# Kernel optimization log

Measured on AMD Instinct MI355X. Metric: run time of the kernel, lower is better.

Reference implementation:

```python
import jax, jax.numpy as jnp
import numpy as np

HIDDEN = 512
CTX = 768
B, N, M = 8, 4096, 1024


def setup_inputs() -> dict:
    key = jax.random.key(0)
    ks = jax.random.split(key, 7)
    s = lambda fan_in: 1.0 / np.sqrt(fan_in)
    return {
        "x": jax.random.normal(ks[0], (B, N, HIDDEN), jnp.float32),
        "context": jax.random.normal(ks[1], (B, M, CTX), jnp.float32),
        "Wq": jax.random.normal(ks[2], (HIDDEN, HIDDEN), jnp.float32) * s(HIDDEN),
        "bq": jnp.zeros((HIDDEN,), jnp.float32),
        "Wk": jax.random.normal(ks[3], (CTX, HIDDEN), jnp.float32) * s(CTX),
        "bk": jnp.zeros((HIDDEN,), jnp.float32),
        "Wv": jax.random.normal(ks[4], (CTX, HIDDEN), jnp.float32) * s(CTX),
        "bv": jnp.zeros((HIDDEN,), jnp.float32),
        "Wo": jax.random.normal(ks[5], (HIDDEN, HIDDEN), jnp.float32) * s(HIDDEN),
        "bo": jnp.zeros((HIDDEN,), jnp.float32),
    }


def reference(x, context, Wq, bq, Wk, bk, Wv, bv, Wo, bo):
    scale = HIDDEN ** (-0.5)
    q = jnp.einsum("bnd,de->bne", x, Wq) + bq          # [B,N,H]
    k = jnp.einsum("bmc,ce->bme", context, Wk) + bk    # [B,M,H]
    v = jnp.einsum("bmc,ce->bme", context, Wv) + bv    # [B,M,H]
    scores = jnp.einsum("bne,bme->bnm", q, k) * scale  # [B,N,M]
    attn = jax.nn.softmax(scores, axis=-1)
    ctx_out = jnp.einsum("bnm,bme->bne", attn, v)      # [B,N,H]
    out = jnp.einsum("bne,ed->bnd", ctx_out, Wo) + bo
    return out + x
```

## Files before the change

### kernel.cpp

```cpp
#include <hip/hip_runtime.h>

typedef __attribute__((ext_vector_type(8))) short short8;
typedef __attribute__((ext_vector_type(4))) float f32x4;
typedef __attribute__((ext_vector_type(4))) int i32x4;

#define NSEQ 4096
#define MSEQ 1024
#define HID  512
#define CTXD 768

static __device__ __forceinline__ unsigned short f2bf(float f) {
  union { float f; unsigned u; } v; v.f = f;
  return (unsigned short)((v.u + 0x7fffu + ((v.u >> 16) & 1u)) >> 16);
}
static __device__ __forceinline__ float bf2f(unsigned short u) {
  union { unsigned u; float f; } v; v.u = ((unsigned)u) << 16;
  return v.f;
}

static __device__ __forceinline__ void gld16(const void* g, void* l) {
  __builtin_amdgcn_global_load_lds((const __attribute__((address_space(1))) void*)g,
                                   (__attribute__((address_space(3))) void*)l, 16, 0, 0);
}

__global__ void k_transpose(const float* __restrict__ W, unsigned short* __restrict__ WT,
                            int K, int N) {
  __shared__ float tile[32][33];
  int k0 = blockIdx.x * 32, n0 = blockIdx.y * 32;
  int tx = threadIdx.x, ty = threadIdx.y;
#pragma unroll
  for (int i = 0; i < 32; i += 8)
    tile[ty + i][tx] = W[(size_t)(k0 + ty + i) * N + n0 + tx];
  __syncthreads();
#pragma unroll
  for (int i = 0; i < 32; i += 8)
    WT[(size_t)(n0 + ty + i) * K + k0 + tx] = f2bf(tile[tx][ty + i]);
}

__global__ void k_cast(const float* __restrict__ in, unsigned short* __restrict__ out, int n8) {
  int i = blockIdx.x * blockDim.x + threadIdx.x;
  int stride = gridDim.x * blockDim.x;
  for (; i < n8; i += stride) {
    f32x4 v0 = *(const f32x4*)(in + (size_t)i * 8);
    f32x4 v1 = *(const f32x4*)(in + (size_t)i * 8 + 4);
    unsigned short tmp[8] __attribute__((aligned(16)));
    tmp[0] = f2bf(v0[0]); tmp[1] = f2bf(v0[1]); tmp[2] = f2bf(v0[2]); tmp[3] = f2bf(v0[3]);
    tmp[4] = f2bf(v1[0]); tmp[5] = f2bf(v1[1]); tmp[6] = f2bf(v1[2]); tmp[7] = f2bf(v1[3]);
    *(i32x4*)(out + (size_t)i * 8) = *(const i32x4*)tmp;
  }
}

template<int BIAS_MODE, bool RES, bool OUT_BF16, int ZMODE>
__global__ __launch_bounds__(256, 2) void k_gemm(
    const unsigned short* __restrict__ A, const unsigned short* __restrict__ B,
    const float* __restrict__ bias, const float* __restrict__ resv,
    void* __restrict__ Cv, int M, int N, int K,
    long sA, long sB, long sC, long sR) {
  __shared__ __align__(16) char lds[65536];
  const int t = threadIdx.x, lane = t & 63, wid = t >> 6;
  const int wr = wid >> 1, wc = wid & 1;
  int m0, n0, z;
  if (ZMODE == 2) {
    int bid = blockIdx.x; z = bid & 7; int r = bid >> 3;
    m0 = (r >> 3) * 128; n0 = (r & 7) * 128;
  } else {
    m0 = blockIdx.x * 128; n0 = blockIdx.y * 128; z = blockIdx.z;
  }
  const unsigned short* Ab = A + (size_t)z * sA;
  const unsigned short* Bb = B + (size_t)z * sB;

  const f32x4 fz = {0.f, 0.f, 0.f, 0.f};
  f32x4 acc[4][4];
#pragma unroll
  for (int i = 0; i < 4; i++)
#pragma unroll
    for (int j = 0; j < 4; j++) acc[i][j] = fz;

  const int srow = t >> 3;
  const int schunk = t & 7;

  auto stage = [&](int kk, int buf) {
    const char* a8 = (const char*)Ab;
    const char* b8 = (const char*)Bb;
#pragma unroll
    for (int i = 0; i < 4; i++) {
      int row = i * 32 + srow;
      gld16(a8 + ((size_t)(m0 + row) * K + kk) * 2 + ((schunk ^ (row & 7)) << 4),
            lds + buf * 32768 + i * 4096 + wid * 1024);
    }
#pragma unroll
    for (int i = 0; i < 4; i++) {
      int row = i * 32 + srow;
      gld16(b8 + ((size_t)(n0 + row) * K + kk) * 2 + ((schunk ^ (row & 7)) << 4),
            lds + buf * 32768 + 16384 + i * 4096 + wid * 1024);
    }
  };

  stage(0, 0);
  int buf = 0;
  for (int kk = 0; kk < K; kk += 64) {
    if (kk + 64 < K) {
      stage(kk + 64, buf ^ 1);
      asm volatile("s_waitcnt vmcnt(8)" ::: "memory");
    } else {
      asm volatile("s_waitcnt vmcnt(0)" ::: "memory");
    }
    __builtin_amdgcn_s_barrier();
    const char* As = lds + buf * 32768;
    const char* Bs = As + 16384;
#pragma unroll
    for (int ks = 0; ks < 2; ks++) {
      short8 af[4], bfr[4];
#pragma unroll
      for (int i = 0; i < 4; i++) {
        int r = wr * 64 + i * 16 + (lane & 15);
        af[i] = *(const short8*)(As + r * 128 +
                 (((unsigned)(ks * 64 + (lane >> 4) * 16)) ^ ((unsigned)(r & 7) << 4)));
      }
#pragma unroll
      for (int i = 0; i < 4; i++) {
        int r = wc * 64 + i * 16 + (lane & 15);
        bfr[i] = *(const short8*)(Bs + r * 128 +
                 (((unsigned)(ks * 64 + (lane >> 4) * 16)) ^ ((unsigned)(r & 7) << 4)));
      }
#pragma unroll
      for (int i = 0; i < 4; i++)
#pragma unroll
        for (int j = 0; j < 4; j++)
          acc[i][j] = __builtin_amdgcn_mfma_f32_16x16x32_bf16(af[i], bfr[j], acc[i][j], 0, 0, 0);
    }
    asm volatile("s_waitcnt lgkmcnt(0)" ::: "memory");
    __builtin_amdgcn_s_barrier();
    buf ^= 1;
  }

  const float* res = RES ? (resv + (size_t)z * sR) : nullptr;
  char* Cb = (char*)Cv + (size_t)z * sC * (OUT_BF16 ? 2 : 4);
#pragma unroll
  for (int i = 0; i < 4; i++) {
#pragma unroll
    for (int jj = 0; jj < 4; jj++) {
      int row = m0 + wr * 64 + i * 16 + (lane >> 4) * 4 + jj;
#pragma unroll
      for (int j = 0; j < 4; j++) {
        int col = n0 + wc * 64 + j * 16 + (lane & 15);
        float v = acc[i][j][jj];
        if (BIAS_MODE == 1) v += bias[col];
        if (BIAS_MODE == 2) v += bias[row];
        if (RES) v += res[(size_t)row * N + col];
        if (OUT_BF16) ((unsigned short*)Cb)[(size_t)row * N + col] = f2bf(v);
        else          ((float*)Cb)[(size_t)row * N + col] = v;
      }
    }
  }
}

template<int BIAS_MODE, bool RES, bool OUT_BF16, int ZMODE, int EPI, bool AF32>
__global__ __launch_bounds__(512, 1) void k_gemm3(
    const unsigned short* __restrict__ A, const unsigned short* __restrict__ B,
    const float* __restrict__ bias, const float* __restrict__ resv,
    void* __restrict__ Cv, int M, int N, int K,
    long sA, long sB, long sC, long sR,
    const float* __restrict__ ps, float* __restrict__ psout) {
  __shared__ __align__(16) char lds[99328];
  const int t = threadIdx.x, lane = t & 63, wid = t >> 6;
  const int wr = wid >> 2, wc = wid & 3;
  const int l15 = lane & 15, g = lane >> 4;
  int m0, n0, z;
  if (ZMODE == 1) {
    int bid = blockIdx.x; z = bid & 7; int r = bid >> 3;
    m0 = (r >> 1) * 256; n0 = (r & 1) * 256;
  } else if (ZMODE == 3) {
    int bid = blockIdx.x; z = bid & 7; int r = bid >> 3;
    m0 = (r >> 2) * 256; n0 = (r & 3) * 256;
  } else {
    m0 = blockIdx.x * 256; n0 = blockIdx.y * 256; z = blockIdx.z;
  }
  const unsigned short* Ab = A + (size_t)z * sA;
  const float* Af = (const float*)A + (size_t)z * sA;
  const unsigned short* Bb = B + (size_t)z * sB;

  float* invb = (float*)(lds + 98304);
  if (EPI == 2) {
    if (t < 256) {
      size_t rr = (size_t)z * 4096 + (m0 + t);
      invb[t] = 1.0f / (ps[rr] + ps[32768 + rr] + ps[65536 + rr] + ps[98304 + rr]);
    }
    __syncthreads();
  }

  const f32x4 fz = {0.f, 0.f, 0.f, 0.f};
  f32x4 acc[8][4];
#pragma unroll
  for (int i = 0; i < 8; i++)
#pragma unroll
    for (int j = 0; j < 4; j++) acc[i][j] = fz;

  int rS[2], cS[2];
#pragma unroll
  for (int u = 0; u < 2; u++) {
    int p = u * 8192 + wid * 1024 + lane * 16;
    int L = p >> 7;
    int q = (p & 127) ^ ((L & 7) << 4);
    rS[u] = 2 * L + (q >> 6);
    cS[u] = q & 63;
  }

  auto stageA = [&](int kk, int buf, int u) {
    gld16((const char*)Ab + ((size_t)(m0 + rS[u]) * K + kk) * 2 + cS[u],
          lds + buf * 32768 + u * 8192 + wid * 1024);
  };
  auto stageB = [&](int kk, int buf, int u) {
    gld16((const char*)Bb + ((size_t)(n0 + rS[u]) * K + kk) * 2 + cS[u],
          lds + buf * 32768 + 16384 + u * 8192 + wid * 1024);
  };

  f32x4 araw[2][2];
  auto loadAraw = [&](int kk) {
#pragma unroll
    for (int u = 0; u < 2; u++) {
      const float* src = Af + (size_t)(m0 + rS[u]) * K + kk + (cS[u] >> 1);
      araw[u][0] = *(const f32x4*)(src);
      araw[u][1] = *(const f32x4*)(src + 4);
    }
  };
  auto writeA = [&](int buf) {
#pragma unroll
    for (int u = 0; u < 2; u++) {
      unsigned short tmp[8] __attribute__((aligned(16)));
#pragma unroll
      for (int e = 0; e < 4; e++) tmp[e] = f2bf(araw[u][0][e]);
#pragma unroll
      for (int e = 0; e < 4; e++) tmp[4 + e] = f2bf(araw[u][1][e]);
      *(i32x4*)(lds + buf * 32768 + u * 8192 + wid * 1024 + lane * 16) = *(const i32x4*)tmp;
    }
  };

  auto ldso = [&](int r, int gg) -> unsigned {
    unsigned L = (unsigned)(r >> 1);
    return L * 128 + ((((unsigned)(r & 1)) * 64 + (unsigned)gg * 16) ^ ((L & 7) << 4));
  };

  const int NT = K >> 5;
  if (AF32) {
    loadAraw(0);
#pragma unroll
    for (int u = 0; u < 2; u++) stageB(0, 0, u);
    writeA(0);
    loadAraw(32);
#pragma unroll
    for (int u = 0; u < 2; u++) stageB(32, 1, u);
    writeA(1);
  } else {
#pragma unroll
    for (int u = 0; u < 2; u++) { stageA(0, 0, u); }
#pragma unroll
    for (int u = 0; u < 2; u++) { stageB(0, 0, u); }
#pragma unroll
    for (int u = 0; u < 2; u++) { stageA(32, 1, u); }
#pragma unroll
    for (int u = 0; u < 2; u++) { stageB(32, 1, u); }
  }

  for (int tt = 0; tt < NT; tt++) {
    if (AF32) {
      asm volatile("s_waitcnt vmcnt(0)" ::: "memory");
    } else if (tt + 1 < NT) {
      asm volatile("s_waitcnt vmcnt(4)" ::: "memory");
    } else {
      asm volatile("s_waitcnt vmcnt(0)" ::: "memory");
    }
    __builtin_amdgcn_s_barrier();
    asm volatile("" ::: "memory");
    const char* As = lds + (tt % 3) * 32768;
    const char* Bs = As + 16384;
    const int kk2 = (tt + 2) << 5;
    const bool st = kk2 < K;
    const int bn = (tt + 2) % 3;

    if (AF32 && st) loadAraw(kk2);

    short8 bfr[4], af[8];
#pragma unroll
    for (int fj = 0; fj < 4; fj++) {
      int r = wc * 64 + fj * 16 + l15;
      bfr[fj] = *(const short8*)(Bs + ldso(r, g));
    }
#pragma unroll
    for (int fi = 0; fi < 8; fi++) {
      int r = wr * 128 + fi * 16 + l15;
      af[fi] = *(const short8*)(As + ldso(r, g));
    }
    if (!AF32 && st) { stageA(kk2, bn, 0); stageA(kk2, bn, 1); stageB(kk2, bn, 0); stageB(kk2, bn, 1); }
    __builtin_amdgcn_s_setprio(1);
#pragma unroll
    for (int fi = 0; fi < 8; fi++)
#pragma unroll
      for (int fj = 0; fj < 4; fj++)
        acc[fi][fj] =
            __builtin_amdgcn_mfma_f32_16x16x32_bf16(af[fi], bfr[fj], acc[fi][fj], 0, 0, 0);
    __builtin_amdgcn_s_setprio(0);
    if (AF32 && st) { writeA(bn); stageB(kk2, bn, 0); stageB(kk2, bn, 1); }
    asm volatile("" ::: "memory");
  }
  asm volatile("s_waitcnt lgkmcnt(0)" ::: "memory");
  __builtin_amdgcn_s_barrier();
  asm volatile("" ::: "memory");

  char* Cb = (char*)Cv + (size_t)z * sC * (OUT_BF16 ? 2 : 4);

  if (EPI == 1) {
    const float scale = 0.044194173824159216f;
    float* redb = (float*)lds;
#pragma unroll
    for (int i = 0; i < 8; i++) {
#pragma unroll
      for (int jj = 0; jj < 4; jj++) {
        int rl = wr * 128 + i * 16 + g * 4 + jj;
        int row = m0 + rl;
        float e4 = 0.f;
#pragma unroll
        for (int j = 0; j < 4; j++) {
          int col = n0 + wc * 64 + j * 16 + l15;
          float e = __expf(acc[i][j][jj] * scale);
          unsigned short h = f2bf(e);
          ((unsigned short*)Cb)[(size_t)row * N + col] = h;
          e4 += bf2f(h);
        }
#pragma unroll
        for (int d = 1; d < 16; d <<= 1) e4 += __shfl_xor(e4, d, 64);
        if (l15 == 0) redb[wc * 256 + rl] = e4;
      }
    }
    __syncthreads();
    if (t < 256) {
      float s4 = redb[t] + redb[256 + t] + redb[512 + t] + redb[768 + t];
      psout[(size_t)(n0 >> 8) * 32768 + (size_t)z * 4096 + (m0 + t)] = s4;
    }
    return;
  }

  const float* res = RES ? (resv + (size_t)z * sR) : nullptr;
#pragma unroll
  for (int i = 0; i < 8; i++) {
#pragma unroll
    for (int jj = 0; jj < 4; jj++) {
      int rl = wr * 128 + i * 16 + g * 4 + jj;
      int row = m0 + rl;
      float inv = 1.0f;
      if (EPI == 2) inv = invb[rl];
#pragma unroll
      for (int j = 0; j < 4; j++) {
        int col = n0 + wc * 64 + j * 16 + l15;
        float v = acc[i][j][jj];
        if (EPI == 2) v *= inv;
        if (BIAS_MODE == 1) v += bias[col];
        if (BIAS_MODE == 2) v += bias[row];
        if (RES) v += res[(size_t)row * N + col];
        if (OUT_BF16) ((unsigned short*)Cb)[(size_t)row * N + col] = f2bf(v);
        else          ((float*)Cb)[(size_t)row * N + col] = v;
      }
    }
  }
}

extern "C" void kernel_launch(void* const* d_in, const int* in_sizes, int n_in,
                              void* d_out, int out_size, void* d_ws, size_t ws_size,
                              hipStream_t stream) {
  (void)in_sizes; (void)n_in; (void)out_size; (void)ws_size;
  const float* x   = (const float*)d_in[0];
  const float* ctx = (const float*)d_in[1];
  const float* Wq  = (const float*)d_in[2];
  const float* bq  = (const float*)d_in[3];
  const float* Wk  = (const float*)d_in[4];
  const float* bk  = (const float*)d_in[5];
  const float* Wv  = (const float*)d_in[6];
  const float* bv  = (const float*)d_in[7];
  const float* Wo  = (const float*)d_in[8];
  const float* bo  = (const float*)d_in[9];
  float* out = (float*)d_out;

  char* ws = (char*)d_ws;
  unsigned short* qb   = (unsigned short*)(ws);
  unsigned short* kbuf = (unsigned short*)(ws + 33554432);
  unsigned short* Vb   = (unsigned short*)(ws + 41943040);
  unsigned short* UT   = (unsigned short*)(ws + 50331648);
  unsigned short* WqT  = (unsigned short*)(ws + 58720256);
  unsigned short* WkT  = (unsigned short*)(ws + 59244544);
  unsigned short* WvT  = (unsigned short*)(ws + 60030976);
  unsigned short* WoT  = (unsigned short*)(ws + 60817408);
  unsigned short* cb   = (unsigned short*)(ws + 61341696);
  unsigned short* Sbuf = (unsigned short*)(ws + 73924608);
  float* psums = (float*)(ws + 141033472);

  dim3 tb(32, 8);
  k_transpose<<<dim3(16, 16), tb, 0, stream>>>(Wq, WqT, 512, 512);
  k_transpose<<<dim3(24, 16), tb, 0, stream>>>(Wk, WkT, 768, 512);
  k_transpose<<<dim3(24, 16), tb, 0, stream>>>(Wv, WvT, 768, 512);
  k_transpose<<<dim3(16, 16), tb, 0, stream>>>(Wo, WoT, 512, 512);

  k_cast<<<dim3(2048), 256, 0, stream>>>(ctx, cb, 786432);

  k_gemm3<1, false, true, 0, 0, true><<<dim3(128, 2, 1), 512, 0, stream>>>(
      (const unsigned short*)x, WqT, bq, nullptr, qb, 32768, 512, 512,
      0, 0, 0, 0, nullptr, nullptr);
  k_gemm<1, false, true, 0><<<dim3(64, 4, 1), 256, 0, stream>>>(
      cb, WkT, bk, nullptr, kbuf, 8192, 512, 768, 0, 0, 0, 0);
  k_gemm<1, false, true, 0><<<dim3(64, 4, 1), 256, 0, stream>>>(
      cb, WvT, bv, nullptr, Vb, 8192, 512, 768, 0, 0, 0, 0);
  k_gemm<0, false, true, 2><<<dim3(256), 256, 0, stream>>>(
      WoT, Vb, nullptr, nullptr, UT, 512, 1024, 512,
      0, (long)1024 * 512, (long)512 * 1024, 0);
  k_gemm3<0, false, true, 3, 1, false><<<dim3(512), 512, 0, stream>>>(
      qb, kbuf, nullptr, nullptr, Sbuf, 4096, 1024, 512,
      (long)4096 * 512, (long)1024 * 512, (long)4096 * 1024, 0, nullptr, psums);
  k_gemm3<1, true, false, 1, 2, false><<<dim3(256), 512, 0, stream>>>(
      Sbuf, UT, bo, x, out, 4096, 512, 1024,
      (long)4096 * 1024, (long)512 * 1024, (long)4096 * 512, (long)4096 * 512,
      psums, nullptr);
}
```

Before: 185.1 us.

## Fuse K/V projections into one fp32-input GEMM and batch weight transposes

Merges the four weight-transpose launches into one z-indexed kernel and drops the separate context bf16 cast kernel. The K and V projections become a single 256-tile GEMM that reads fp32 context directly and writes an interleaved [B*M,1024] K|V buffer. A leading-dimension parameter (ldb) is added so downstream GEMMs can read K and V out of that interleaved buffer. This removes several launches and a full cast pass over the context. The cost is two device memcpys to concatenate the biases and a strided B-operand layout for the attention GEMMs.

```diff
diff --git a/kernel.cpp b/kernel.cpp
--- a/kernel.cpp
+++ b/kernel.cpp
@@ -23,10 +23,20 @@
                                    (__attribute__((address_space(3))) void*)l, 16, 0, 0);
 }
 
-__global__ void k_transpose(const float* __restrict__ W, unsigned short* __restrict__ WT,
-                            int K, int N) {
+__global__ void k_transpose4(const float* __restrict__ W0, const float* __restrict__ W1,
+                             const float* __restrict__ W2, const float* __restrict__ W3,
+                             unsigned short* __restrict__ T0, unsigned short* __restrict__ T1,
+                             unsigned short* __restrict__ T2, unsigned short* __restrict__ T3) {
   __shared__ float tile[32][33];
+  const int zz = blockIdx.z;
+  const float* W; unsigned short* T; int K;
+  if (zz == 0)      { W = W0; T = T0; K = 512; }
+  else if (zz == 1) { W = W1; T = T1; K = 768; }
+  else if (zz == 2) { W = W2; T = T2; K = 768; }
+  else              { W = W3; T = T3; K = 512; }
   int k0 = blockIdx.x * 32, n0 = blockIdx.y * 32;
+  if (k0 >= K) return;
+  const int N = 512;
   int tx = threadIdx.x, ty = threadIdx.y;
 #pragma unroll
   for (int i = 0; i < 32; i += 8)
@@ -34,20 +44,7 @@
   __syncthreads();
 #pragma unroll
   for (int i = 0; i < 32; i += 8)
-    WT[(size_t)(n0 + ty + i) * K + k0 + tx] = f2bf(tile[tx][ty + i]);
-}
-
-__global__ void k_cast(const float* __restrict__ in, unsigned short* __restrict__ out, int n8) {
-  int i = blockIdx.x * blockDim.x + threadIdx.x;
-  int stride = gridDim.x * blockDim.x;
-  for (; i < n8; i += stride) {
-    f32x4 v0 = *(const f32x4*)(in + (size_t)i * 8);
-    f32x4 v1 = *(const f32x4*)(in + (size_t)i * 8 + 4);
-    unsigned short tmp[8] __attribute__((aligned(16)));
-    tmp[0] = f2bf(v0[0]); tmp[1] = f2bf(v0[1]); tmp[2] = f2bf(v0[2]); tmp[3] = f2bf(v0[3]);
-    tmp[4] = f2bf(v1[0]); tmp[5] = f2bf(v1[1]); tmp[6] = f2bf(v1[2]); tmp[7] = f2bf(v1[3]);
-    *(i32x4*)(out + (size_t)i * 8) = *(const i32x4*)tmp;
-  }
+    T[(size_t)(n0 + ty + i) * K + k0 + tx] = f2bf(tile[tx][ty + i]);
 }
 
 template<int BIAS_MODE, bool RES, bool OUT_BF16, int ZMODE>
@@ -55,7 +52,7 @@
     const unsigned short* __restrict__ A, const unsigned short* __restrict__ B,
     const float* __restrict__ bias, const float* __restrict__ resv,
     void* __restrict__ Cv, int M, int N, int K,
-    long sA, long sB, long sC, long sR) {
+    long sA, long sB, long sC, long sR, long ldb) {
   __shared__ __align__(16) char lds[65536];
   const int t = threadIdx.x, lane = t & 63, wid = t >> 6;
   const int wr = wid >> 1, wc = wid & 1;
@@ -91,7 +88,7 @@
 #pragma unroll
     for (int i = 0; i < 4; i++) {
       int row = i * 32 + srow;
-      gld16(b8 + ((size_t)(n0 + row) * K + kk) * 2 + ((schunk ^ (row & 7)) << 4),
+      gld16(b8 + ((size_t)(n0 + row) * ldb + kk) * 2 + ((schunk ^ (row & 7)) << 4),
             lds + buf * 32768 + 16384 + i * 4096 + wid * 1024);
     }
   };
@@ -160,7 +157,7 @@
     const unsigned short* __restrict__ A, const unsigned short* __restrict__ B,
     const float* __restrict__ bias, const float* __restrict__ resv,
     void* __restrict__ Cv, int M, int N, int K,
-    long sA, long sB, long sC, long sR,
+    long sA, long sB, long sC, long sR, long ldb,
     const float* __restrict__ ps, float* __restrict__ psout) {
   __shared__ __align__(16) char lds[99328];
   const int t = threadIdx.x, lane = t & 63, wid = t >> 6;
@@ -211,7 +208,7 @@
           lds + buf * 32768 + u * 8192 + wid * 1024);
   };
   auto stageB = [&](int kk, int buf, int u) {
-    gld16((const char*)Bb + ((size_t)(n0 + rS[u]) * K + kk) * 2 + cS[u],
+    gld16((const char*)Bb + ((size_t)(n0 + rS[u]) * ldb + kk) * 2 + cS[u],
           lds + buf * 32768 + 16384 + u * 8192 + wid * 1024);
   };
 
@@ -382,40 +379,37 @@
 
   char* ws = (char*)d_ws;
   unsigned short* qb   = (unsigned short*)(ws);
-  unsigned short* kbuf = (unsigned short*)(ws + 33554432);
-  unsigned short* Vb   = (unsigned short*)(ws + 41943040);
+  unsigned short* kv   = (unsigned short*)(ws + 33554432);
   unsigned short* UT   = (unsigned short*)(ws + 50331648);
   unsigned short* WqT  = (unsigned short*)(ws + 58720256);
   unsigned short* WkT  = (unsigned short*)(ws + 59244544);
   unsigned short* WvT  = (unsigned short*)(ws + 60030976);
   unsigned short* WoT  = (unsigned short*)(ws + 60817408);
-  unsigned short* cb   = (unsigned short*)(ws + 61341696);
-  unsigned short* Sbuf = (unsigned short*)(ws + 73924608);
-  float* psums = (float*)(ws + 141033472);
-
-  dim3 tb(32, 8);
-  k_transpose<<<dim3(16, 16), tb, 0, stream>>>(Wq, WqT, 512, 512);
-  k_transpose<<<dim3(24, 16), tb, 0, stream>>>(Wk, WkT, 768, 512);
-  k_transpose<<<dim3(24, 16), tb, 0, stream>>>(Wv, WvT, 768, 512);
-  k_transpose<<<dim3(16, 16), tb, 0, stream>>>(Wo, WoT, 512, 512);
-
-  k_cast<<<dim3(2048), 256, 0, stream>>>(ctx, cb, 786432);
+  float* bkv           = (float*)(ws + 61341696);
+  unsigned short* Sbuf = (unsigned short*)(ws + 61345792);
+  float* psums         = (float*)(ws + 128454656);
+
+  hipMemcpyAsync(bkv, bk, 512 * sizeof(float), hipMemcpyDeviceToDevice, stream);
+  hipMemcpyAsync(bkv + 512, bv, 512 * sizeof(float), hipMemcpyDeviceToDevice, stream);
+
+  k_transpose4<<<dim3(24, 16, 4), dim3(32, 8), 0, stream>>>(
+      Wq, Wk, Wv, Wo, WqT, WkT, WvT, WoT);
 
   k_gemm3<1, false, true, 0, 0, true><<<dim3(128, 2, 1), 512, 0, stream>>>(
       (const unsigned short*)x, WqT, bq, nullptr, qb, 32768, 512, 512,
-      0, 0, 0, 0, nullptr, nullptr);
-  k_gemm<1, false, true, 0><<<dim3(64, 4, 1), 256, 0, stream>>>(
-      cb, WkT, bk, nullptr, kbuf, 8192, 512, 768, 0, 0, 0, 0);
-  k_gemm<1, false, true, 0><<<dim3(64, 4, 1), 256, 0, stream>>>(
-      cb, WvT, bv, nullptr, Vb, 8192, 512, 768, 0, 0, 0, 0);
+      0, 0, 0, 0, 512, nullptr, nullptr);
+  k_gemm3<1, false, true, 0, 0, true><<<dim3(32, 4, 1), 512, 0, stream>>>(
+      (const unsigned short*)ctx, WkT, bkv, nullptr, kv, 8192, 1024, 768,
+      0, 0, 0, 0, 768, nullptr, nullptr);
   k_gemm<0, false, true, 2><<<dim3(256), 256, 0, stream>>>(
-      WoT, Vb, nullptr, nullptr, UT, 512, 1024, 512,
-      0, (long)1024 * 512, (long)512 * 1024, 0);
+      WoT, kv + 512, nullptr, nullptr, UT, 512, 1024, 512,
+      0, (long)1024 * 1024, (long)512 * 1024, 0, 1024);
   k_gemm3<0, false, true, 3, 1, false><<<dim3(512), 512, 0, stream>>>(
-      qb, kbuf, nullptr, nullptr, Sbuf, 4096, 1024, 512,
-      (long)4096 * 512, (long)1024 * 512, (long)4096 * 1024, 0, nullptr, psums);
+      qb, kv, nullptr, nullptr, Sbuf, 4096, 1024, 512,
+      (long)4096 * 512, (long)1024 * 1024, (long)4096 * 1024, 0, 1024,
+      nullptr, psums);
   k_gemm3<1, true, false, 1, 2, false><<<dim3(256), 512, 0, stream>>>(
       Sbuf, UT, bo, x, out, 4096, 512, 1024,
-      (long)4096 * 1024, (long)512 * 1024, (long)4096 * 512, (long)4096 * 512,
+      (long)4096 * 1024, (long)512 * 1024, (long)4096 * 512, (long)4096 * 512, 1024,
       psums, nullptr);
 }
```

Result: slower. 191.1 us (+3.2%).
